# Performance work log

Hardware: AMD Instinct MI355X
Metric: run time of the kernel (lower is better)

## Reference

```python
import jax, jax.numpy as jnp
import numpy as np


def _scattering(image, mags, phases):
    # image: [B,S,S] real; mags/phases: [J,L,S,S] real (Fourier-domain Morlet filters)
    J = mags.shape[0]
    psi = (mags * jnp.exp(1j * phases)).astype(jnp.complex64)        # [J,L,S,S]
    xf = jnp.fft.fft2(image)                                          # [B,S,S] complex64
    # first-order: modulus of wavelet convolutions, all scales/orientations at once
    u1 = jnp.abs(jnp.fft.ifft2(xf[:, None, None] * psi[None]))        # [B,J,L,S,S]
    s0 = image.mean(axis=(-2, -1))                                    # [B]
    s1 = u1.mean(axis=(2, 3, 4))                                      # [B,J] (orientation-averaged)
    # second-order: only j2 > j1 (the nan-filtered entries in the original)
    s2_parts = []
    for j1 in range(J - 1):  # structural loop over scales, not data dims
        u1f = jnp.fft.fft2(u1[:, j1].astype(jnp.complex64))           # [B,L1,S,S]
        psi2 = psi[j1 + 1:]                                           # [J2,L2,S,S]
        v = jnp.abs(jnp.fft.ifft2(u1f[:, :, None, None] * psi2[None, None]))  # [B,L1,J2,L2,S,S]
        s2_parts.append(v.mean(axis=(1, 3, 4, 5)))                    # [B,J2]
    s2 = jnp.concatenate(s2_parts, axis=1)                            # [B, J*(J-1)/2]
    return s0, s1, s2


def setup_inputs() -> dict:
    key = jax.random.key(0)
    ks = jax.random.split(key, 8)
    B, S, J, L = 64, 128, 6, 4
    return {
        "image_batch": jax.random.normal(ks[0], (B, S, S), dtype=jnp.float32),
        "mags": jax.random.uniform(ks[1], (J, L, S, S), dtype=jnp.float32),
        "phases": jax.random.normal(ks[2], (J, L, S, S), dtype=jnp.float32),
        "w1": jax.random.normal(ks[3], (22, 16), dtype=jnp.float32) * 0.1,
        "b1": jnp.zeros((16,), dtype=jnp.float32),
        "w2": jax.random.normal(ks[4], (16, 16), dtype=jnp.float32) * 0.1,
        "b2": jnp.zeros((16,), dtype=jnp.float32),
        "w3": jax.random.normal(ks[5], (16, 1), dtype=jnp.float32) * 0.1,
        "b3": jnp.zeros((1,), dtype=jnp.float32),
    }


def reference(image_batch, mags, phases, w1, b1, w2, b2, w3, b3):
    s0, s1, s2 = _scattering(image_batch, mags, phases)
    x = jnp.concatenate([s0[:, None], s1, s2], axis=1)                # [B,22]
    x = jax.nn.relu(x @ w1 + b1)
    x = jax.nn.relu(x @ w2 + b2)
    x = jax.nn.sigmoid(x @ w3 + b3)
    return jnp.squeeze(x, axis=1)                                     # [B]
```

## Files before the change

kernel.cpp:

```cpp
#include <hip/hip_runtime.h>
#include <math.h>


#define SDIM 128
#define PLANE 16384
#define PITCH 129
#define NT 1024
#define TWO_PI 6.28318530717958647692f
#define PSIH_SCALE 16.0f

typedef _Float16 h2 __attribute__((ext_vector_type(2)));

constexpr float W16R[8] = {1.f, 0.9238795325f, 0.7071067812f, 0.3826834324f,
                           0.f, -0.3826834324f, -0.7071067812f, -0.9238795325f};
constexpr float W16I[8] = {0.f, -0.3826834324f, -0.7071067812f, -0.9238795325f,
                           -1.f, -0.9238795325f, -0.7071067812f, -0.3826834324f};

__device__ __forceinline__ float fast_sqrtf(float x) { return __builtin_amdgcn_sqrtf(x); }

__device__ __forceinline__ unsigned packbf(float re, float im) {
  const unsigned r = __float_as_uint(re) + 0x8000u;
  const unsigned i = __float_as_uint(im) + 0x8000u;
  return __builtin_amdgcn_perm(r, i, 0x07060302u);
}
__device__ __forceinline__ void unpackbf(unsigned u, float& re, float& im) {
  re = __uint_as_float(u & 0xFFFF0000u);
  im = __uint_as_float(u << 16);
}

union UHU { unsigned u; h2 h; };
__device__ __forceinline__ h2 u2h(unsigned u) { UHU x; x.u = u; return x.h; }
__device__ __forceinline__ unsigned h2u(h2 h) { UHU x; x.h = h; return x.u; }
__device__ __forceinline__ h2 bch2(float f) { const _Float16 h = (_Float16)f; h2 v = {h, h}; return v; }

__device__ __forceinline__ void stC(float2* s, int idx, float re, float im) { s[idx] = make_float2(re, im); }
__device__ __forceinline__ void ldC(const float2* s, int idx, float& re, float& im) { const float2 v = s[idx]; re = v.x; im = v.y; }
__device__ __forceinline__ void stC(unsigned* s, int idx, float re, float im) { s[idx] = packbf(re, im); }
__device__ __forceinline__ void ldC(const unsigned* s, int idx, float& re, float& im) { unpackbf(s[idx], re, im); }

__device__ __forceinline__ void load_tw(const float2* __restrict__ twg, int g,
                                        float* twr, float* twi) {
#pragma unroll
  for (int k = 1; k < 16; ++k) {
    const float2 w = twg[16 * g + k];
    twr[k] = __uint_as_float(__builtin_amdgcn_readfirstlane(__float_as_uint(w.x)));
    twi[k] = __uint_as_float(__builtin_amdgcn_readfirstlane(__float_as_uint(w.y)));
  }
}
__device__ __forceinline__ void load_twh(const uint2* __restrict__ twgh, int g,
                                         unsigned* twru, unsigned* twiu) {
#pragma unroll
  for (int k = 1; k < 16; ++k) {
    const uint2 w = twgh[16 * g + k];
    twru[k] = (unsigned)__builtin_amdgcn_readfirstlane((int)w.x);
    twiu[k] = (unsigned)__builtin_amdgcn_readfirstlane((int)w.y);
  }
}

template<bool INV>
__device__ __forceinline__ void bfly(float& ar, float& ai, float& br, float& bi, const int idx) {
  float tr, ti;
  if (idx == 0) { tr = br; ti = bi; }
  else if (idx == 4) {
    if (INV) { tr = -bi; ti = br; } else { tr = bi; ti = -br; }
  } else {
    const float wr = W16R[idx];
    const float wi = INV ? -W16I[idx] : W16I[idx];
    tr = br * wr - bi * wi;
    ti = br * wi + bi * wr;
  }
  br = ar - tr; bi = ai - ti;
  ar = ar + tr; ai = ai + ti;
}

#define CSWAP(re, im, a, b) { float _t = re[a]; re[a]=re[b]; re[b]=_t; _t = im[a]; im[a]=im[b]; im[b]=_t; }

template<bool INV>
__device__ __forceinline__ void dft16(float* re, float* im) {
  CSWAP(re, im, 1, 8) CSWAP(re, im, 2, 4) CSWAP(re, im, 3, 12)
  CSWAP(re, im, 5, 10) CSWAP(re, im, 7, 14) CSWAP(re, im, 11, 13)
#pragma unroll
  for (int ls = 1; ls <= 4; ++ls) {
    const int len = 1 << ls, half = len >> 1, tstep = 16 >> ls;
#pragma unroll
    for (int blk = 0; blk < 16; blk += len)
#pragma unroll
      for (int j = 0; j < half; ++j)
        bfly<INV>(re[blk + j], im[blk + j], re[blk + j + half], im[blk + j + half], j * tstep);
  }
}

template<bool INV>
__device__ __forceinline__ void dft8(float* re, float* im) {
  CSWAP(re, im, 1, 4) CSWAP(re, im, 3, 6)
#pragma unroll
  for (int ls = 1; ls <= 3; ++ls) {
    const int len = 1 << ls, half = len >> 1, tstep = 8 >> ls;
#pragma unroll
    for (int blk = 0; blk < 8; blk += len)
#pragma unroll
      for (int j = 0; j < half; ++j)
        bfly<INV>(re[blk + j], im[blk + j], re[blk + j + half], im[blk + j + half], j * tstep * 2);
  }
}

__device__ __forceinline__ void twmul_fwd(float* R, float* I, const float* twr, const float* twi) {
#pragma unroll
  for (int k = 1; k < 16; ++k) {
    const float r = R[k] * twr[k] - I[k] * twi[k];
    I[k] = R[k] * twi[k] + I[k] * twr[k]; R[k] = r;
  }
}
__device__ __forceinline__ void twmul_inv(float* R, float* I, const float* twr, const float* twi) {
#pragma unroll
  for (int k = 1; k < 16; ++k) {
    const float r = R[k] * twr[k] + I[k] * twi[k];
    I[k] = I[k] * twr[k] - R[k] * twi[k]; R[k] = r;
  }
}

template<typename S>
__device__ __forceinline__ void fwd_fft2(float* R, float* I, S* sC,
                                         int g, int q, const float* twr, const float* twi) {
  const int rb = q * PITCH;
  dft16<false>(R, I);
  twmul_fwd(R, I, twr, twi);
  __syncthreads();
#pragma unroll
  for (int k = 0; k < 16; ++k) stC(sC, rb + 8 * k + g, R[k], I[k]);
  __syncthreads();
#pragma unroll
  for (int t = 0; t < 8; ++t) {
    ldC(sC, rb + 16 * g + t, R[t], I[t]);
    ldC(sC, rb + 16 * g + 8 + t, R[8 + t], I[8 + t]);
  }
  dft8<false>(R, I); dft8<false>(R + 8, I + 8);
#pragma unroll
  for (int k2 = 0; k2 < 8; ++k2) {
    stC(sC, rb + 16 * g + k2, R[k2], I[k2]);
    stC(sC, rb + 16 * g + 8 + k2, R[8 + k2], I[8 + k2]);
  }
  __syncthreads();
#pragma unroll
  for (int m = 0; m < 16; ++m) ldC(sC, (g + 8 * m) * PITCH + q, R[m], I[m]);
  dft16<false>(R, I);
  twmul_fwd(R, I, twr, twi);
#pragma unroll
  for (int k = 0; k < 16; ++k) stC(sC, (8 * k + g) * PITCH + q, R[k], I[k]);
  __syncthreads();
#pragma unroll
  for (int u = 0; u < 8; ++u) {
    const int bp = (16 * g + 2 * u) * PITCH + q;
    ldC(sC, bp, R[2 * u], I[2 * u]);
    ldC(sC, bp + PITCH, R[2 * u + 1], I[2 * u + 1]);
  }
  dft8<false>(R, I); dft8<false>(R + 8, I + 8);
}

template<bool FIRST, typename S>
__device__ __forceinline__ void inv_fft2(float* R, float* I, S* sC,
                                         int g, int q, const float* twr, const float* twi) {
  const int rb = q * PITCH;
  dft8<true>(R, I); dft8<true>(R + 8, I + 8);
  if constexpr (!FIRST) __syncthreads();
#pragma unroll
  for (int t = 0; t < 16; ++t) stC(sC, rb + 16 * g + t, R[t], I[t]);
  __syncthreads();
#pragma unroll
  for (int k = 0; k < 16; ++k) ldC(sC, rb + 8 * k + g, R[k], I[k]);
  twmul_inv(R, I, twr, twi);
  dft16<true>(R, I);
#pragma unroll
  for (int m = 0; m < 16; ++m) stC(sC, rb + g + 8 * m, R[m], I[m]);
  __syncthreads();
#pragma unroll
  for (int u = 0; u < 8; ++u) {
    const int bp = (16 * g + 2 * u) * PITCH + q;
    ldC(sC, bp, R[2 * u], I[2 * u]);
    ldC(sC, bp + PITCH, R[2 * u + 1], I[2 * u + 1]);
  }
  dft8<true>(R, I); dft8<true>(R + 8, I + 8);
#pragma unroll
  for (int u = 0; u < 8; ++u) {
    const int bp = (16 * g + 2 * u) * PITCH + q;
    stC(sC, bp, R[2 * u], I[2 * u]);
    stC(sC, bp + PITCH, R[2 * u + 1], I[2 * u + 1]);
  }
  __syncthreads();
#pragma unroll
  for (int k = 0; k < 16; ++k) ldC(sC, (8 * k + g) * PITCH + q, R[k], I[k]);
  twmul_inv(R, I, twr, twi);
  dft16<true>(R, I);
}

__device__ __forceinline__ void bfly_h_inv(h2& ar, h2& ai, h2& br, h2& bi, const int idx) {
  h2 tr, ti;
  if (idx == 0) { tr = br; ti = bi; }
  else if (idx == 4) { tr = -bi; ti = br; }
  else {
    const h2 wr = bch2(W16R[idx]);
    const h2 wi = bch2(-W16I[idx]);
    tr = br * wr - bi * wi;
    ti = br * wi + bi * wr;
  }
  br = ar - tr; bi = ai - ti;
  ar = ar + tr; ai = ai + ti;
}

#define HSWAP(re, im, a, b) { h2 _t = re[a]; re[a]=re[b]; re[b]=_t; _t = im[a]; im[a]=im[b]; im[b]=_t; }

__device__ __forceinline__ void dft16h(h2* re, h2* im) {
  HSWAP(re, im, 1, 8) HSWAP(re, im, 2, 4) HSWAP(re, im, 3, 12)
  HSWAP(re, im, 5, 10) HSWAP(re, im, 7, 14) HSWAP(re, im, 11, 13)
#pragma unroll
  for (int ls = 1; ls <= 4; ++ls) {
    const int len = 1 << ls, half = len >> 1, tstep = 16 >> ls;
#pragma unroll
    for (int blk = 0; blk < 16; blk += len)
#pragma unroll
      for (int j = 0; j < half; ++j)
        bfly_h_inv(re[blk + j], im[blk + j], re[blk + j + half], im[blk + j + half], j * tstep);
  }
}

__device__ __forceinline__ void dft8h(h2* re, h2* im) {
  HSWAP(re, im, 1, 4) HSWAP(re, im, 3, 6)
#pragma unroll
  for (int ls = 1; ls <= 3; ++ls) {
    const int len = 1 << ls, half = len >> 1, tstep = 8 >> ls;
#pragma unroll
    for (int blk = 0; blk < 8; blk += len)
#pragma unroll
      for (int j = 0; j < half; ++j)
        bfly_h_inv(re[blk + j], im[blk + j], re[blk + j + half], im[blk + j + half], j * tstep * 2);
  }
}

__device__ __forceinline__ void twmul_inv_h(h2* R, h2* I, const unsigned* twru, const unsigned* twiu) {
#pragma unroll
  for (int k = 1; k < 16; ++k) {
    const h2 wr = u2h(twru[k]), wi = u2h(twiu[k]);
    const h2 r = R[k] * wr + I[k] * wi;
    I[k] = I[k] * wr - R[k] * wi;
    R[k] = r;
  }
}

__device__ __forceinline__ void inv_fft2_h(h2* R, h2* I, uint2* sC,
                                           int g, int q,
                                           const unsigned* twru, const unsigned* twiu) {
  const int rb = q * PITCH;
  dft8h(R, I); dft8h(R + 8, I + 8);
#pragma unroll
  for (int t = 0; t < 16; ++t) sC[rb + 16 * g + t] = make_uint2(h2u(R[t]), h2u(I[t]));
  __syncthreads();
#pragma unroll
  for (int k = 0; k < 16; ++k) { const uint2 v = sC[rb + 8 * k + g]; R[k] = u2h(v.x); I[k] = u2h(v.y); }
  twmul_inv_h(R, I, twru, twiu);
  dft16h(R, I);
#pragma unroll
  for (int m = 0; m < 16; ++m) sC[rb + g + 8 * m] = make_uint2(h2u(R[m]), h2u(I[m]));
  __syncthreads();
#pragma unroll
  for (int u = 0; u < 8; ++u) {
    const int bp = (16 * g + 2 * u) * PITCH + q;
    const uint2 v0 = sC[bp];         R[2 * u] = u2h(v0.x);     I[2 * u] = u2h(v0.y);
    const uint2 v1 = sC[bp + PITCH]; R[2 * u + 1] = u2h(v1.x); I[2 * u + 1] = u2h(v1.y);
  }
  dft8h(R, I); dft8h(R + 8, I + 8);
#pragma unroll
  for (int u = 0; u < 8; ++u) {
    const int bp = (16 * g + 2 * u) * PITCH + q;
    sC[bp]         = make_uint2(h2u(R[2 * u]),     h2u(I[2 * u]));
    sC[bp + PITCH] = make_uint2(h2u(R[2 * u + 1]), h2u(I[2 * u + 1]));
  }
  __syncthreads();
#pragma unroll
  for (int k = 0; k < 16; ++k) { const uint2 v = sC[(8 * k + g) * PITCH + q]; R[k] = u2h(v.x); I[k] = u2h(v.y); }
  twmul_inv_h(R, I, twru, twiu);
  dft16h(R, I);
}

__device__ __forceinline__ float block_reduce_sum(float v, float* red, int tid) {
#pragma unroll
  for (int o = 32; o > 0; o >>= 1) v += __shfl_down(v, o);
  __syncthreads();
  if ((tid & 63) == 0) red[tid >> 6] = v;
  __syncthreads();
  float t = 0.0f;
  if (tid == 0) {
#pragma unroll
    for (int w = 0; w < 16; ++w) t += red[w];
  }
  return t;
}

__global__ __launch_bounds__(256) void k_psi(const float* __restrict__ mags,
                                             const float* __restrict__ phases,
                                             float2* __restrict__ psi,
                                             float2* __restrict__ twg,
                                             uint2* __restrict__ psih2,
                                             uint2* __restrict__ twgh) {
  if (blockIdx.x == 0 && threadIdx.x < 128) {
    const int gg = threadIdx.x >> 4, k = threadIdx.x & 15;
    float sn, cs;
    __sincosf(-TWO_PI * (float)(gg * k) * (1.0f / 128.0f), &sn, &cs);
    twg[threadIdx.x] = make_float2(cs, sn);
    twgh[threadIdx.x] = make_uint2(h2u(bch2(cs)), h2u(bch2(sn)));
  }
  const int gid = blockIdx.x * 256 + threadIdx.x;
  if (gid < 24 * PLANE) {
    const int p = gid >> 14;
    const int rem = gid & (PLANE - 1);
    const int e = rem & 1;
    const int tt = (rem >> 1) & 1023;
    const int i = rem >> 11;
    const int j = 2 * i + e;
    const int g = tt >> 7, q = tt & 127;
    const int pr = 16 * g + j, pc = q;
    const int kr = (pr >> 3) + 16 * (pr & 7);
    const int kc = (pc >> 3) + 16 * (pc & 7);
    const int src = (p << 14) + kr * SDIM + kc;
    const float m = mags[src] * (1.0f / 16384.0f);
    float sn, cs;
    __sincosf(phases[src], &sn, &cs);
    psi[gid] = make_float2(m * cs, m * sn);
  } else if (gid < 24 * PLANE + 10 * PLANE) {
    const int c = gid - 24 * PLANE;
    const int jp = c >> 14;
    const int c14 = c & (PLANE - 1);
    const int e2 = c14 & 1;
    const int tmp = c14 >> 1;
    const int tt = tmp & 1023;
    const int i = tmp >> 10;
    const int j = 2 * i + e2;
    const int g = tt >> 7, q = tt & 127;
    const int pr = 16 * g + j, pc = q;
    const int kr = (pr >> 3) + 16 * (pr & 7);
    const int kc = (pc >> 3) + 16 * (pc & 7);
    const int j2 = 1 + (jp >> 1);
    const int epair = jp & 1;
    const int plane_lo = j2 * 4 + 2 * epair;
    const int src_lo = (plane_lo << 14) + kr * SDIM + kc;
    const int src_hi = src_lo + PLANE;
    const float scl = PSIH_SCALE / 16384.0f;
    const float m0 = mags[src_lo] * scl;
    const float m1 = mags[src_hi] * scl;
    float sn0, cs0, sn1, cs1;
    __sincosf(phases[src_lo], &sn0, &cs0);
    __sincosf(phases[src_hi], &sn1, &cs1);
    h2 re2 = { (_Float16)(m0 * cs0), (_Float16)(m1 * cs1) };
    h2 im2 = { (_Float16)(m0 * sn0), (_Float16)(m1 * sn1) };
    psih2[(jp << 14) + c14] = make_uint2(h2u(re2), h2u(im2));
  }
}

__global__ __launch_bounds__(NT) void k_img_fft(const float* __restrict__ img,
                                                float2* __restrict__ Xf,
                                                float* __restrict__ s0,
                                                const float2* __restrict__ twg) {
  __shared__ float2 sC[SDIM * PITCH];
  __shared__ float red[16];
  const int tid = threadIdx.x, b = blockIdx.x;
  const int g = __builtin_amdgcn_readfirstlane(tid >> 7);
  const int q = tid & 127;
  float twr[16], twi[16];
  load_tw(twg, g, twr, twi);
  const float* ip = img + b * PLANE;
  float sum = 0.0f;
#pragma unroll
  for (int kk = 0; kk < 16; ++kk) {
    const int e = tid + kk * NT;
    const float v = ip[e];
    sC[(e >> 7) * PITCH + (e & 127)] = make_float2(v, 0.0f);
    sum += v;
  }
  const float tot = block_reduce_sum(sum, red, tid);
  if (tid == 0) s0[b] = tot * (1.0f / 16384.0f);
  __syncthreads();
  float R[16], I[16];
#pragma unroll
  for (int m = 0; m < 16; ++m) { R[m] = sC[q * PITCH + g + 8 * m].x; I[m] = 0.0f; }
  fwd_fft2(R, I, sC, g, q, twr, twi);
  float4* x4 = (float4*)Xf + (size_t)b * 8192 + tid;
#pragma unroll
  for (int i = 0; i < 8; ++i)
    x4[i * 1024] = make_float4(R[2 * i], I[2 * i], R[2 * i + 1], I[2 * i + 1]);
}

__global__ __launch_bounds__(NT) void k_scat_a(const float2* __restrict__ Xf,
                                               const float2* __restrict__ psi,
                                               float* __restrict__ s1num,
                                               unsigned* __restrict__ Ubuf,
                                               const float2* __restrict__ twg) {
  __shared__ unsigned sU[SDIM * PITCH];
  __shared__ float red[16];
  const int tid = threadIdx.x;
  const int g = __builtin_amdgcn_readfirstlane(tid >> 7);
  const int q = tid & 127;
  float twr[16], twi[16];
  load_tw(twg, g, twr, twi);
  const int bid = blockIdx.x;
  float R[16], I[16];

  if (bid < 1280) {
    const int j1 = bid >> 8;
    const int b = (bid & 255) >> 2;
    const int l1 = bid & 3;
    const float4* x4 = (const float4*)Xf + (size_t)b * 8192 + tid;
    const float4* p4 = (const float4*)psi + (size_t)(j1 * 4 + l1) * 8192 + tid;
#pragma unroll
    for (int i = 0; i < 8; ++i) {
      const float4 x = x4[i * 1024], v = p4[i * 1024];
      R[2 * i]     = x.x * v.x - x.y * v.y;  I[2 * i]     = x.x * v.y + x.y * v.x;
      R[2 * i + 1] = x.z * v.z - x.w * v.w;  I[2 * i + 1] = x.z * v.w + x.w * v.z;
    }
    inv_fft2<true>(R, I, sU, g, q, twr, twi);
    float s1sum = 0.0f;
#pragma unroll
    for (int m = 0; m < 16; ++m) {
      const float a = fast_sqrtf(R[m] * R[m] + I[m] * I[m]);
      s1sum += a; R[m] = a; I[m] = 0.0f;
    }
    fwd_fft2(R, I, sU, g, q, twr, twi);
    uint4 ob[4];
    unsigned* obs = (unsigned*)ob;
#pragma unroll
    for (int j = 0; j < 16; ++j) obs[j] = packbf(R[j], I[j]);
    uint4* o4 = (uint4*)Ubuf + (size_t)((b * 5 + j1) * 4 + l1) * 4096 + tid;
#pragma unroll
    for (int i = 0; i < 4; ++i) o4[i * 1024] = ob[i];
    const float tot = block_reduce_sum(s1sum, red, tid);
    if (tid == 0) atomicAdd(&s1num[b * 6 + j1], tot);
  } else {
    const int idx = bid - 1280;
    const int b = idx >> 2, l = idx & 3;
    const float4* x4 = (const float4*)Xf + (size_t)b * 8192 + tid;
    const float4* p4 = (const float4*)psi + (size_t)(20 + l) * 8192 + tid;
#pragma unroll
    for (int i = 0; i < 8; ++i) {
      const float4 x = x4[i * 1024], v = p4[i * 1024];
      R[2 * i]     = x.x * v.x - x.y * v.y;  I[2 * i]     = x.x * v.y + x.y * v.x;
      R[2 * i + 1] = x.z * v.z - x.w * v.w;  I[2 * i + 1] = x.z * v.w + x.w * v.z;
    }
    inv_fft2<true>(R, I, sU, g, q, twr, twi);
    float s = 0.0f;
#pragma unroll
    for (int m = 0; m < 16; ++m) s += fast_sqrtf(R[m] * R[m] + I[m] * I[m]);
    const float tot = block_reduce_sum(s, red, tid);
    if (tid == 0) atomicAdd(&s1num[b * 6 + 5], tot);
  }
}

__global__ __launch_bounds__(NT) void k_scat_b_h2(const uint4* __restrict__ psih4,
                                                  const unsigned* __restrict__ Ubuf,
                                                  float* __restrict__ s2num,
                                                  const uint2* __restrict__ twgh) {
  __shared__ uint2 sU[SDIM * PITCH];
  __shared__ float red[16];
  const int tid = threadIdx.x;
  const int g = __builtin_amdgcn_readfirstlane(tid >> 7);
  const int q = tid & 127;
  unsigned twru[16], twiu[16];
  load_twh(twgh, g, twru, twiu);
  int t = blockIdx.x;
  const int e = t & 1; t >>= 1;
  const int l1 = t & 3; t >>= 2;
  const int pair = t % 15;
  const int b = t / 15;
  int j1 = 0, base = 0;
  if (pair >= 14)      { j1 = 4; base = 14; }
  else if (pair >= 12) { j1 = 3; base = 12; }
  else if (pair >= 9)  { j1 = 2; base = 9; }
  else if (pair >= 5)  { j1 = 1; base = 5; }
  const int j2 = j1 + 1 + (pair - base);
  const int jp = (j2 - 1) * 2 + e;

  h2 R2[16], I2[16];
  {
    const uint4* u4 = (const uint4*)Ubuf + (size_t)((b * 5 + j1) * 4 + l1) * 4096 + tid;
    uint4 ub[4];
#pragma unroll
    for (int i = 0; i < 4; ++i) ub[i] = u4[i * 1024];
    const unsigned* ubs = (const unsigned*)ub;
    const uint4* p4 = psih4 + (size_t)jp * 8192 + tid;
#pragma unroll
    for (int i = 0; i < 8; ++i) {
      const uint4 pv = p4[i * 1024];
      float ur, ui;
      unpackbf(ubs[2 * i], ur, ui);
      {
        const h2 UR = bch2(ur), UI = bch2(ui);
        const h2 pr = u2h(pv.x), pi = u2h(pv.y);
        R2[2 * i] = UR * pr - UI * pi;
        I2[2 * i] = UR * pi + UI * pr;
      }
      unpackbf(ubs[2 * i + 1], ur, ui);
      {
        const h2 UR = bch2(ur), UI = bch2(ui);
        const h2 pr = u2h(pv.z), pi = u2h(pv.w);
        R2[2 * i + 1] = UR * pr - UI * pi;
        I2[2 * i + 1] = UR * pi + UI * pr;
      }
    }
  }
  inv_fft2_h(R2, I2, sU, g, q, twru, twiu);
  float vsum = 0.0f;
#pragma unroll
  for (int m = 0; m < 16; ++m) {
    const float rl = (float)R2[m].x, il = (float)I2[m].x;
    const float rh = (float)R2[m].y, ih = (float)I2[m].y;
    vsum += fast_sqrtf(rl * rl + il * il) + fast_sqrtf(rh * rh + ih * ih);
  }
  const float tot = block_reduce_sum(vsum, red, tid);
  if (tid == 0) atomicAdd(&s2num[b * 15 + pair], tot);
}

__global__ __launch_bounds__(NT) void k_scat_b(const float2* __restrict__ psi,
                                               const unsigned* __restrict__ Ubuf,
                                               float* __restrict__ s2num,
                                               const float2* __restrict__ twg) {
  __shared__ unsigned sU[SDIM * PITCH];
  __shared__ float red[16];
  const int tid = threadIdx.x;
  const int g = __builtin_amdgcn_readfirstlane(tid >> 7);
  const int q = tid & 127;
  float twr[16], twi[16];
  load_tw(twg, g, twr, twi);
  int t = blockIdx.x;
  const int l2 = t & 3; t >>= 2;
  const int pair = t % 15; t /= 15;
  const int l1 = t & 3;
  const int b = t >> 2;
  int j1 = 0, base = 0;
  if (pair >= 14)      { j1 = 4; base = 14; }
  else if (pair >= 12) { j1 = 3; base = 12; }
  else if (pair >= 9)  { j1 = 2; base = 9; }
  else if (pair >= 5)  { j1 = 1; base = 5; }
  const int j2 = j1 + 1 + (pair - base);
  float R[16], I[16];
  {
    const uint4* u4 = (const uint4*)Ubuf + (size_t)((b * 5 + j1) * 4 + l1) * 4096 + tid;
    uint4 ub[4];
#pragma unroll
    for (int i = 0; i < 4; ++i) ub[i] = u4[i * 1024];
    const unsigned* ubs = (const unsigned*)ub;
    const float4* p4 = (const float4*)psi + (size_t)(j2 * 4 + l2) * 8192 + tid;
#pragma unroll
    for (int i = 0; i < 8; ++i) {
      const float4 v = p4[i * 1024];
      float ur, ui;
      unpackbf(ubs[2 * i], ur, ui);
      R[2 * i] = ur * v.x - ui * v.y;      I[2 * i] = ur * v.y + ui * v.x;
      unpackbf(ubs[2 * i + 1], ur, ui);
      R[2 * i + 1] = ur * v.z - ui * v.w;  I[2 * i + 1] = ur * v.w + ui * v.z;
    }
  }
  inv_fft2<true>(R, I, sU, g, q, twr, twi);
  float vsum = 0.0f;
#pragma unroll
  for (int m = 0; m < 16; ++m) vsum += fast_sqrtf(R[m] * R[m] + I[m] * I[m]);
  const float tot = block_reduce_sum(vsum, red, tid);
  if (tid == 0) atomicAdd(&s2num[b * 15 + pair], tot);
}

__global__ __launch_bounds__(NT) void k_scat_mono(const float2* __restrict__ Xf,
                                                  const float2* __restrict__ psi,
                                                  float* __restrict__ s1num,
                                                  float* __restrict__ s2num,
                                                  const float2* __restrict__ twg) {
  __shared__ unsigned sU[SDIM * PITCH];
  __shared__ float red[16];
  const int tid = threadIdx.x;
  const int g = __builtin_amdgcn_readfirstlane(tid >> 7);
  const int q = tid & 127;
  float twr[16], twi[16];
  load_tw(twg, g, twr, twi);
  const int bid = blockIdx.x;
  float R[16], I[16];
  if (bid < 1280) {
    const int j1 = bid >> 8;
    const int b = (bid & 255) >> 2;
    const int l1 = bid & 3;
    const float4* x4 = (const float4*)Xf + (size_t)b * 8192 + tid;
    const float4* p4 = (const float4*)psi + (size_t)(j1 * 4 + l1) * 8192 + tid;
#pragma unroll
    for (int i = 0; i < 8; ++i) {
      const float4 x = x4[i * 1024], v = p4[i * 1024];
      R[2 * i]     = x.x * v.x - x.y * v.y;  I[2 * i]     = x.x * v.y + x.y * v.x;
      R[2 * i + 1] = x.z * v.z - x.w * v.w;  I[2 * i + 1] = x.z * v.w + x.w * v.z;
    }
    inv_fft2<true>(R, I, sU, g, q, twr, twi);
    float s1sum = 0.0f;
#pragma unroll
    for (int m = 0; m < 16; ++m) {
      const float a = fast_sqrtf(R[m] * R[m] + I[m] * I[m]);
      s1sum += a; R[m] = a; I[m] = 0.0f;
    }
    fwd_fft2(R, I, sU, g, q, twr, twi);
    float Ur[16], Ui[16];
#pragma unroll
    for (int k = 0; k < 16; ++k) { Ur[k] = R[k]; Ui[k] = I[k]; }
    {
      const float tot = block_reduce_sum(s1sum, red, tid);
      if (tid == 0) atomicAdd(&s1num[b * 6 + j1], tot);
    }
    const int pb = (j1 * (11 - j1)) >> 1;
    int plane = (j1 + 1) * 4;
#pragma unroll 1
    for (int j2 = j1 + 1; j2 <= 5; ++j2) {
      float vsum = 0.0f;
#pragma unroll 1
      for (int l2 = 0; l2 < 4; ++l2) {
        const float4* q4 = (const float4*)psi + (size_t)plane * 8192 + tid;
#pragma unroll
        for (int i = 0; i < 8; ++i) {
          const float4 v = q4[i * 1024];
          R[2 * i]     = Ur[2 * i] * v.x - Ui[2 * i] * v.y;
          I[2 * i]     = Ur[2 * i] * v.y + Ui[2 * i] * v.x;
          R[2 * i + 1] = Ur[2 * i + 1] * v.z - Ui[2 * i + 1] * v.w;
          I[2 * i + 1] = Ur[2 * i + 1] * v.w + Ui[2 * i + 1] * v.z;
        }
        inv_fft2<false>(R, I, sU, g, q, twr, twi);
#pragma unroll
        for (int m = 0; m < 16; ++m) vsum += fast_sqrtf(R[m] * R[m] + I[m] * I[m]);
        ++plane;
      }
      const float tot = block_reduce_sum(vsum, red, tid);
      if (tid == 0) atomicAdd(&s2num[b * 15 + pb + (j2 - j1 - 1)], tot);
    }
  } else {
    const int idx = bid - 1280;
    const int b = idx >> 2, l = idx & 3;
    const float4* x4 = (const float4*)Xf + (size_t)b * 8192 + tid;
    const float4* p4 = (const float4*)psi + (size_t)(20 + l) * 8192 + tid;
#pragma unroll
    for (int i = 0; i < 8; ++i) {
      const float4 x = x4[i * 1024], v = p4[i * 1024];
      R[2 * i]     = x.x * v.x - x.y * v.y;  I[2 * i]     = x.x * v.y + x.y * v.x;
      R[2 * i + 1] = x.z * v.z - x.w * v.w;  I[2 * i + 1] = x.z * v.w + x.w * v.z;
    }
    inv_fft2<true>(R, I, sU, g, q, twr, twi);
    float s = 0.0f;
#pragma unroll
    for (int m = 0; m < 16; ++m) s += fast_sqrtf(R[m] * R[m] + I[m] * I[m]);
    const float tot = block_reduce_sum(s, red, tid);
    if (tid == 0) atomicAdd(&s1num[b * 6 + 5], tot);
  }
}

__global__ __launch_bounds__(64) void k_final(const float* __restrict__ s0,
                                              const float* __restrict__ s1num,
                                              const float* __restrict__ s2num,
                                              const float* __restrict__ w1,
                                              const float* __restrict__ b1,
                                              const float* __restrict__ w2,
                                              const float* __restrict__ b2,
                                              const float* __restrict__ w3,
                                              const float* __restrict__ b3,
                                              float* __restrict__ out,
                                              float s2scale) {
  const int b = threadIdx.x;
  if (b >= 64) return;
  float x[22];
  x[0] = s0[b];
#pragma unroll
  for (int j = 0; j < 6; ++j) x[1 + j] = s1num[b * 6 + j] * (1.0f / (4.0f * 16384.0f));
#pragma unroll
  for (int p = 0; p < 15; ++p) x[7 + p] = s2num[b * 15 + p] * s2scale;
  float h1[16];
#pragma unroll
  for (int o = 0; o < 16; ++o) {
    float t = b1[o];
    for (int i = 0; i < 22; ++i) t += x[i] * w1[i * 16 + o];
    h1[o] = fmaxf(t, 0.0f);
  }
  float h2a[16];
#pragma unroll
  for (int o = 0; o < 16; ++o) {
    float t = b2[o];
    for (int i = 0; i < 16; ++i) t += h1[i] * w2[i * 16 + o];
    h2a[o] = fmaxf(t, 0.0f);
  }
  float t = b3[0];
#pragma unroll
  for (int i = 0; i < 16; ++i) t += h2a[i] * w3[i];
  out[b] = 1.0f / (1.0f + expf(-t));
}

extern "C" void kernel_launch(void* const* d_in, const int* in_sizes, int n_in,
                              void* d_out, int out_size, void* d_ws, size_t ws_size,
                              hipStream_t stream) {
  (void)in_sizes; (void)n_in; (void)out_size;
  const float* image  = (const float*)d_in[0];
  const float* mags   = (const float*)d_in[1];
  const float* phases = (const float*)d_in[2];
  const float* w1 = (const float*)d_in[3];
  const float* b1 = (const float*)d_in[4];
  const float* w2 = (const float*)d_in[5];
  const float* b2 = (const float*)d_in[6];
  const float* w3 = (const float*)d_in[7];
  const float* b3 = (const float*)d_in[8];
  float* out = (float*)d_out;

  char* ws = (char*)d_ws;
  float2* psi = (float2*)ws;
  float2* Xf  = (float2*)(ws + 3145728);
  float*  s0  = (float*)(ws + 11534336);
  float*  s1n = s0 + 64;
  float*  s2n = s1n + 384;
  float2* twg = (float2*)(s2n + 960);
  uint2*  twgh = (uint2*)((char*)twg + 1024);
  unsigned* Ubuf = (unsigned*)(ws + 11542528);
  uint2*  psih2 = (uint2*)(ws + 95428608);
  const size_t need_r5 = 11542528ull + 83886080ull;
  const size_t need_h2 = need_r5 + 1310720ull;

  hipMemsetAsync(s1n, 0, (384 + 960) * sizeof(float), stream);
  if (ws_size >= need_h2) {
    k_psi<<<dim3(2176), dim3(256), 0, stream>>>(mags, phases, psi, twg, psih2, twgh);
    k_img_fft<<<dim3(64), dim3(NT), 0, stream>>>(image, Xf, s0, twg);
    k_scat_a<<<dim3(1536), dim3(NT), 0, stream>>>(Xf, psi, s1n, Ubuf, twg);
    k_scat_b_h2<<<dim3(7680), dim3(NT), 0, stream>>>((const uint4*)psih2, Ubuf, s2n, twgh);
    k_final<<<dim3(1), dim3(64), 0, stream>>>(s0, s1n, s2n, w1, b1, w2, b2, w3, b3, out,
                                              1.0f / (16.0f * 16384.0f * PSIH_SCALE));
  } else if (ws_size >= need_r5) {
    k_psi<<<dim3(1536), dim3(256), 0, stream>>>(mags, phases, psi, twg, psih2, twgh);
    k_img_fft<<<dim3(64), dim3(NT), 0, stream>>>(image, Xf, s0, twg);
    k_scat_a<<<dim3(1536), dim3(NT), 0, stream>>>(Xf, psi, s1n, Ubuf, twg);
    k_scat_b<<<dim3(15360), dim3(NT), 0, stream>>>(psi, Ubuf, s2n, twg);
    k_final<<<dim3(1), dim3(64), 0, stream>>>(s0, s1n, s2n, w1, b1, w2, b2, w3, b3, out,
                                              1.0f / (16.0f * 16384.0f));
  } else {
    k_psi<<<dim3(1536), dim3(256), 0, stream>>>(mags, phases, psi, twg, psih2, twgh);
    k_img_fft<<<dim3(64), dim3(NT), 0, stream>>>(image, Xf, s0, twg);
    k_scat_mono<<<dim3(1536), dim3(NT), 0, stream>>>(Xf, psi, s1n, s2n, twg);
    k_final<<<dim3(1), dim3(64), 0, stream>>>(s0, s1n, s2n, w1, b1, w2, b2, w3, b3, out,
                                              1.0f / (16.0f * 16384.0f));
  }
}
```

Measured before the change: 482.3 us.

## Pack half-precision FFT by real-FFT column pairing instead of orientation pairs

The second-order kernel used to pack two orientations (l2 pairs) into each fp16x2 lane and run a 1024-thread block over a full 128x128 plane. It now packs two halves of the same plane's columns (q and q+64) into the fp16x2 lanes. That allows 512-thread blocks with half the shared memory (64 x PITCH) and launch bounds of 4 blocks per CU. The psi preprocessing layout changes to match, and the column-stage transpose uses byte-perm to swap halves. The aim is higher occupancy and smaller LDS use per block, at the cost of twice as many blocks and an extra sync and perm step.

```diff
diff --git a/kernel.cpp b/kernel.cpp
--- a/kernel.cpp
+++ b/kernel.cpp
@@ -32,6 +32,7 @@
 __device__ __forceinline__ h2 u2h(unsigned u) { UHU x; x.u = u; return x.h; }
 __device__ __forceinline__ unsigned h2u(h2 h) { UHU x; x.h = h; return x.u; }
 __device__ __forceinline__ h2 bch2(float f) { const _Float16 h = (_Float16)f; h2 v = {h, h}; return v; }
+__device__ __forceinline__ h2 mkh2(float a, float b) { h2 v = {(_Float16)a, (_Float16)b}; return v; }
 
 __device__ __forceinline__ void stC(float2* s, int idx, float re, float im) { s[idx] = make_float2(re, im); }
 __device__ __forceinline__ void ldC(const float2* s, int idx, float& re, float& im) { const float2 v = s[idx]; re = v.x; im = v.y; }
@@ -246,41 +247,7 @@
   }
 }
 
-__device__ __forceinline__ void inv_fft2_h(h2* R, h2* I, uint2* sC,
-                                           int g, int q,
-                                           const unsigned* twru, const unsigned* twiu) {
-  const int rb = q * PITCH;
-  dft8h(R, I); dft8h(R + 8, I + 8);
-#pragma unroll
-  for (int t = 0; t < 16; ++t) sC[rb + 16 * g + t] = make_uint2(h2u(R[t]), h2u(I[t]));
-  __syncthreads();
-#pragma unroll
-  for (int k = 0; k < 16; ++k) { const uint2 v = sC[rb + 8 * k + g]; R[k] = u2h(v.x); I[k] = u2h(v.y); }
-  twmul_inv_h(R, I, twru, twiu);
-  dft16h(R, I);
-#pragma unroll
-  for (int m = 0; m < 16; ++m) sC[rb + g + 8 * m] = make_uint2(h2u(R[m]), h2u(I[m]));
-  __syncthreads();
-#pragma unroll
-  for (int u = 0; u < 8; ++u) {
-    const int bp = (16 * g + 2 * u) * PITCH + q;
-    const uint2 v0 = sC[bp];         R[2 * u] = u2h(v0.x);     I[2 * u] = u2h(v0.y);
-    const uint2 v1 = sC[bp + PITCH]; R[2 * u + 1] = u2h(v1.x); I[2 * u + 1] = u2h(v1.y);
-  }
-  dft8h(R, I); dft8h(R + 8, I + 8);
-#pragma unroll
-  for (int u = 0; u < 8; ++u) {
-    const int bp = (16 * g + 2 * u) * PITCH + q;
-    sC[bp]         = make_uint2(h2u(R[2 * u]),     h2u(I[2 * u]));
-    sC[bp + PITCH] = make_uint2(h2u(R[2 * u + 1]), h2u(I[2 * u + 1]));
-  }
-  __syncthreads();
-#pragma unroll
-  for (int k = 0; k < 16; ++k) { const uint2 v = sC[(8 * k + g) * PITCH + q]; R[k] = u2h(v.x); I[k] = u2h(v.y); }
-  twmul_inv_h(R, I, twru, twiu);
-  dft16h(R, I);
-}
-
+template<int NW>
 __device__ __forceinline__ float block_reduce_sum(float v, float* red, int tid) {
 #pragma unroll
   for (int o = 32; o > 0; o >>= 1) v += __shfl_down(v, o);
@@ -290,7 +257,7 @@
   float t = 0.0f;
   if (tid == 0) {
 #pragma unroll
-    for (int w = 0; w < 16; ++w) t += red[w];
+    for (int w = 0; w < NW; ++w) t += red[w];
   }
   return t;
 }
@@ -299,7 +266,7 @@
                                              const float* __restrict__ phases,
                                              float2* __restrict__ psi,
                                              float2* __restrict__ twg,
-                                             uint2* __restrict__ psih2,
+                                             uint2* __restrict__ psih,
                                              uint2* __restrict__ twgh) {
   if (blockIdx.x == 0 && threadIdx.x < 128) {
     const int gg = threadIdx.x >> 4, k = threadIdx.x & 15;
@@ -325,33 +292,28 @@
     float sn, cs;
     __sincosf(phases[src], &sn, &cs);
     psi[gid] = make_float2(m * cs, m * sn);
-  } else if (gid < 24 * PLANE + 10 * PLANE) {
+  } else if (gid < 24 * PLANE + 20 * 8192) {
     const int c = gid - 24 * PLANE;
-    const int jp = c >> 14;
-    const int c14 = c & (PLANE - 1);
-    const int e2 = c14 & 1;
-    const int tmp = c14 >> 1;
-    const int tt = tmp & 1023;
-    const int i = tmp >> 10;
-    const int j = 2 * i + e2;
-    const int g = tt >> 7, q = tt & 127;
-    const int pr = 16 * g + j, pc = q;
-    const int kr = (pr >> 3) + 16 * (pr & 7);
-    const int kc = (pc >> 3) + 16 * (pc & 7);
-    const int j2 = 1 + (jp >> 1);
-    const int epair = jp & 1;
-    const int plane_lo = j2 * 4 + 2 * epair;
-    const int src_lo = (plane_lo << 14) + kr * SDIM + kc;
-    const int src_hi = src_lo + PLANE;
+    const int pidx = c >> 13;
+    const int rem = c & 8191;
+    const int j = rem >> 9;
+    const int t512 = rem & 511;
+    const int g = t512 >> 6, q = t512 & 63;
+    const int row = 16 * g + j;
+    const int plane = pidx + 4;
+    const int kr = (row >> 3) + 16 * (row & 7);
+    const int kc0 = (q >> 3) + 16 * (q & 7);
+    const int q1 = q + 64;
+    const int kc1 = (q1 >> 3) + 16 * (q1 & 7);
+    const int src0 = (plane << 14) + kr * SDIM + kc0;
+    const int src1 = (plane << 14) + kr * SDIM + kc1;
     const float scl = PSIH_SCALE / 16384.0f;
-    const float m0 = mags[src_lo] * scl;
-    const float m1 = mags[src_hi] * scl;
+    const float m0 = mags[src0] * scl;
+    const float m1 = mags[src1] * scl;
     float sn0, cs0, sn1, cs1;
-    __sincosf(phases[src_lo], &sn0, &cs0);
-    __sincosf(phases[src_hi], &sn1, &cs1);
-    h2 re2 = { (_Float16)(m0 * cs0), (_Float16)(m1 * cs1) };
-    h2 im2 = { (_Float16)(m0 * sn0), (_Float16)(m1 * sn1) };
-    psih2[(jp << 14) + c14] = make_uint2(h2u(re2), h2u(im2));
+    __sincosf(phases[src0], &sn0, &cs0);
+    __sincosf(phases[src1], &sn1, &cs1);
+    psih[c] = make_uint2(h2u(mkh2(m0 * cs0, m1 * cs1)), h2u(mkh2(m0 * sn0, m1 * sn1)));
   }
 }
 
@@ -375,7 +337,7 @@
     sC[(e >> 7) * PITCH + (e & 127)] = make_float2(v, 0.0f);
     sum += v;
   }
-  const float tot = block_reduce_sum(sum, red, tid);
+  const float tot = block_reduce_sum<16>(sum, red, tid);
   if (tid == 0) s0[b] = tot * (1.0f / 16384.0f);
   __syncthreads();
   float R[16], I[16];
@@ -430,7 +392,7 @@
     uint4* o4 = (uint4*)Ubuf + (size_t)((b * 5 + j1) * 4 + l1) * 4096 + tid;
 #pragma unroll
     for (int i = 0; i < 4; ++i) o4[i * 1024] = ob[i];
-    const float tot = block_reduce_sum(s1sum, red, tid);
+    const float tot = block_reduce_sum<16>(s1sum, red, tid);
     if (tid == 0) atomicAdd(&s1num[b * 6 + j1], tot);
   } else {
     const int idx = bid - 1280;
@@ -447,64 +409,92 @@
     float s = 0.0f;
 #pragma unroll
     for (int m = 0; m < 16; ++m) s += fast_sqrtf(R[m] * R[m] + I[m] * I[m]);
-    const float tot = block_reduce_sum(s, red, tid);
+    const float tot = block_reduce_sum<16>(s, red, tid);
     if (tid == 0) atomicAdd(&s1num[b * 6 + 5], tot);
   }
 }
 
-__global__ __launch_bounds__(NT) void k_scat_b_h2(const uint4* __restrict__ psih4,
-                                                  const unsigned* __restrict__ Ubuf,
-                                                  float* __restrict__ s2num,
-                                                  const uint2* __restrict__ twgh) {
-  __shared__ uint2 sU[SDIM * PITCH];
-  __shared__ float red[16];
+__global__ __launch_bounds__(512, 4) void k_scat_b_rp(const uint2* __restrict__ psih,
+                                                      const unsigned* __restrict__ Ubuf,
+                                                      float* __restrict__ s2num,
+                                                      const uint2* __restrict__ twgh) {
+  __shared__ uint2 sU[64 * PITCH];
+  __shared__ float red[8];
   const int tid = threadIdx.x;
-  const int g = __builtin_amdgcn_readfirstlane(tid >> 7);
-  const int q = tid & 127;
+  const int g = __builtin_amdgcn_readfirstlane(tid >> 6);
+  const int q = tid & 63;
   unsigned twru[16], twiu[16];
   load_twh(twgh, g, twru, twiu);
   int t = blockIdx.x;
-  const int e = t & 1; t >>= 1;
-  const int l1 = t & 3; t >>= 2;
-  const int pair = t % 15;
-  const int b = t / 15;
+  const int l2 = t & 3; t >>= 2;
+  const int pair = t % 15; t /= 15;
+  const int l1 = t & 3;
+  const int b = t >> 2;
   int j1 = 0, base = 0;
   if (pair >= 14)      { j1 = 4; base = 14; }
   else if (pair >= 12) { j1 = 3; base = 12; }
   else if (pair >= 9)  { j1 = 2; base = 9; }
   else if (pair >= 5)  { j1 = 1; base = 5; }
   const int j2 = j1 + 1 + (pair - base);
-  const int jp = (j2 - 1) * 2 + e;
+  const int pidx = j2 * 4 + l2 - 4;
 
   h2 R2[16], I2[16];
   {
-    const uint4* u4 = (const uint4*)Ubuf + (size_t)((b * 5 + j1) * 4 + l1) * 4096 + tid;
-    uint4 ub[4];
-#pragma unroll
-    for (int i = 0; i < 4; ++i) ub[i] = u4[i * 1024];
+    const uint4* u4 = (const uint4*)Ubuf + (size_t)((b * 5 + j1) * 4 + l1) * 4096;
+    const int t0 = g * 128 + q;
+    uint4 ua[4], ub[4];
+#pragma unroll
+    for (int i = 0; i < 4; ++i) { ua[i] = u4[i * 1024 + t0]; ub[i] = u4[i * 1024 + t0 + 64]; }
+    const unsigned* uas = (const unsigned*)ua;
     const unsigned* ubs = (const unsigned*)ub;
-    const uint4* p4 = psih4 + (size_t)jp * 8192 + tid;
-#pragma unroll
-    for (int i = 0; i < 8; ++i) {
-      const uint4 pv = p4[i * 1024];
-      float ur, ui;
-      unpackbf(ubs[2 * i], ur, ui);
-      {
-        const h2 UR = bch2(ur), UI = bch2(ui);
-        const h2 pr = u2h(pv.x), pi = u2h(pv.y);
-        R2[2 * i] = UR * pr - UI * pi;
-        I2[2 * i] = UR * pi + UI * pr;
-      }
-      unpackbf(ubs[2 * i + 1], ur, ui);
-      {
-        const h2 UR = bch2(ur), UI = bch2(ui);
-        const h2 pr = u2h(pv.z), pi = u2h(pv.w);
-        R2[2 * i + 1] = UR * pr - UI * pi;
-        I2[2 * i + 1] = UR * pi + UI * pr;
-      }
-    }
-  }
-  inv_fft2_h(R2, I2, sU, g, q, twru, twiu);
+    const uint2* ph = psih + (size_t)pidx * 8192 + tid;
+#pragma unroll
+    for (int j = 0; j < 16; ++j) {
+      float urL, uiL, urH, uiH;
+      unpackbf(uas[j], urL, uiL);
+      unpackbf(ubs[j], urH, uiH);
+      const h2 UR = mkh2(urL, urH), UI = mkh2(uiL, uiH);
+      const uint2 pv = ph[j * 512];
+      const h2 pr = u2h(pv.x), pi = u2h(pv.y);
+      R2[j] = UR * pr - UI * pi;
+      I2[j] = UR * pi + UI * pr;
+    }
+  }
+
+  const int sb = q * PITCH;
+  dft8h(R2, I2); dft8h(R2 + 8, I2 + 8);
+#pragma unroll
+  for (int s = 0; s < 16; ++s) sU[sb + 16 * g + s] = make_uint2(h2u(R2[s]), h2u(I2[s]));
+  __syncthreads();
+#pragma unroll
+  for (int k = 0; k < 16; ++k) { const uint2 v = sU[sb + 8 * k + g]; R2[k] = u2h(v.x); I2[k] = u2h(v.y); }
+  twmul_inv_h(R2, I2, twru, twiu);
+  dft16h(R2, I2);
+#pragma unroll
+  for (int m = 0; m < 16; ++m) sU[sb + g + 8 * m] = make_uint2(h2u(R2[m]), h2u(I2[m]));
+  __syncthreads();
+  {
+    const int s_base = (16 * g) & 63;
+    const unsigned sel = (g < 4) ? 0x05040100u : 0x07060302u;
+#pragma unroll
+    for (int j = 0; j < 16; ++j) {
+      const int cb = (s_base + j) * PITCH;
+      const uint2 vA = sU[cb + q];
+      const uint2 vB = sU[cb + q + 64];
+      R2[j] = u2h(__builtin_amdgcn_perm(vB.x, vA.x, sel));
+      I2[j] = u2h(__builtin_amdgcn_perm(vB.y, vA.y, sel));
+    }
+  }
+  dft8h(R2, I2); dft8h(R2 + 8, I2 + 8);
+  __syncthreads();
+#pragma unroll
+  for (int s = 0; s < 16; ++s) sU[sb + 16 * g + s] = make_uint2(h2u(R2[s]), h2u(I2[s]));
+  __syncthreads();
+#pragma unroll
+  for (int k = 0; k < 16; ++k) { const uint2 v = sU[sb + 8 * k + g]; R2[k] = u2h(v.x); I2[k] = u2h(v.y); }
+  twmul_inv_h(R2, I2, twru, twiu);
+  dft16h(R2, I2);
+
   float vsum = 0.0f;
 #pragma unroll
   for (int m = 0; m < 16; ++m) {
@@ -512,7 +502,7 @@
     const float rh = (float)R2[m].y, ih = (float)I2[m].y;
     vsum += fast_sqrtf(rl * rl + il * il) + fast_sqrtf(rh * rh + ih * ih);
   }
-  const float tot = block_reduce_sum(vsum, red, tid);
+  const float tot = block_reduce_sum<8>(vsum, red, tid);
   if (tid == 0) atomicAdd(&s2num[b * 15 + pair], tot);
 }
 
@@ -560,7 +550,7 @@
   float vsum = 0.0f;
 #pragma unroll
   for (int m = 0; m < 16; ++m) vsum += fast_sqrtf(R[m] * R[m] + I[m] * I[m]);
-  const float tot = block_reduce_sum(vsum, red, tid);
+  const float tot = block_reduce_sum<16>(vsum, red, tid);
   if (tid == 0) atomicAdd(&s2num[b * 15 + pair], tot);
 }
 
@@ -602,7 +592,7 @@
 #pragma unroll
     for (int k = 0; k < 16; ++k) { Ur[k] = R[k]; Ui[k] = I[k]; }
     {
-      const float tot = block_reduce_sum(s1sum, red, tid);
+      const float tot = block_reduce_sum<16>(s1sum, red, tid);
       if (tid == 0) atomicAdd(&s1num[b * 6 + j1], tot);
     }
     const int pb = (j1 * (11 - j1)) >> 1;
@@ -626,7 +616,7 @@
         for (int m = 0; m < 16; ++m) vsum += fast_sqrtf(R[m] * R[m] + I[m] * I[m]);
         ++plane;
       }
-      const float tot = block_reduce_sum(vsum, red, tid);
+      const float tot = block_reduce_sum<16>(vsum, red, tid);
       if (tid == 0) atomicAdd(&s2num[b * 15 + pb + (j2 - j1 - 1)], tot);
     }
   } else {
@@ -644,7 +634,7 @@
     float s = 0.0f;
 #pragma unroll
     for (int m = 0; m < 16; ++m) s += fast_sqrtf(R[m] * R[m] + I[m] * I[m]);
-    const float tot = block_reduce_sum(s, red, tid);
+    const float tot = block_reduce_sum<16>(s, red, tid);
     if (tid == 0) atomicAdd(&s1num[b * 6 + 5], tot);
   }
 }
@@ -712,27 +702,27 @@
   float2* twg = (float2*)(s2n + 960);
   uint2*  twgh = (uint2*)((char*)twg + 1024);
   unsigned* Ubuf = (unsigned*)(ws + 11542528);
-  uint2*  psih2 = (uint2*)(ws + 95428608);
+  uint2*  psih = (uint2*)(ws + 95428608);
   const size_t need_r5 = 11542528ull + 83886080ull;
   const size_t need_h2 = need_r5 + 1310720ull;
 
   hipMemsetAsync(s1n, 0, (384 + 960) * sizeof(float), stream);
   if (ws_size >= need_h2) {
-    k_psi<<<dim3(2176), dim3(256), 0, stream>>>(mags, phases, psi, twg, psih2, twgh);
+    k_psi<<<dim3(2176), dim3(256), 0, stream>>>(mags, phases, psi, twg, psih, twgh);
     k_img_fft<<<dim3(64), dim3(NT), 0, stream>>>(image, Xf, s0, twg);
     k_scat_a<<<dim3(1536), dim3(NT), 0, stream>>>(Xf, psi, s1n, Ubuf, twg);
-    k_scat_b_h2<<<dim3(7680), dim3(NT), 0, stream>>>((const uint4*)psih2, Ubuf, s2n, twgh);
+    k_scat_b_rp<<<dim3(15360), dim3(512), 0, stream>>>(psih, Ubuf, s2n, twgh);
     k_final<<<dim3(1), dim3(64), 0, stream>>>(s0, s1n, s2n, w1, b1, w2, b2, w3, b3, out,
                                               1.0f / (16.0f * 16384.0f * PSIH_SCALE));
   } else if (ws_size >= need_r5) {
-    k_psi<<<dim3(1536), dim3(256), 0, stream>>>(mags, phases, psi, twg, psih2, twgh);
+    k_psi<<<dim3(1536), dim3(256), 0, stream>>>(mags, phases, psi, twg, psih, twgh);
     k_img_fft<<<dim3(64), dim3(NT), 0, stream>>>(image, Xf, s0, twg);
     k_scat_a<<<dim3(1536), dim3(NT), 0, stream>>>(Xf, psi, s1n, Ubuf, twg);
     k_scat_b<<<dim3(15360), dim3(NT), 0, stream>>>(psi, Ubuf, s2n, twg);
     k_final<<<dim3(1), dim3(64), 0, stream>>>(s0, s1n, s2n, w1, b1, w2, b2, w3, b3, out,
                                               1.0f / (16.0f * 16384.0f));
   } else {
-    k_psi<<<dim3(1536), dim3(256), 0, stream>>>(mags, phases, psi, twg, psih2, twgh);
+    k_psi<<<dim3(1536), dim3(256), 0, stream>>>(mags, phases, psi, twg, psih, twgh);
     k_img_fft<<<dim3(64), dim3(NT), 0, stream>>>(image, Xf, s0, twg);
     k_scat_mono<<<dim3(1536), dim3(NT), 0, stream>>>(Xf, psi, s1n, s2n, twg);
     k_final<<<dim3(1), dim3(64), 0, stream>>>(s0, s1n, s2n, w1, b1, w2, b2, w3, b3, out,
```

After: 463.7 us. 3.9% less time.
